# Optimization experiments

Measured on AMD Instinct MI355X. Metric: run time of the kernel, lower is better.

Reference implementation:

```python
import jax, jax.numpy as jnp
import numpy as np

B, S, E, H, DK, DV, DF = 4, 2048, 512, 8, 64, 64, 2048
EPS = 1e-3  # keras LayerNormalization default epsilon


def setup_inputs() -> dict:
    key = jax.random.key(0)
    ks = jax.random.split(key, 24)
    def n(k, shape, scale=0.02):
        return jax.random.normal(k, shape, jnp.float32) * scale
    inp = {}
    inp["x"] = jax.random.normal(ks[0], (B, S, E), jnp.float32)
    inp["encoder_output"] = jax.random.normal(ks[1], (B, S, E), jnp.float32)
    # lookahead mask: 1 above the diagonal (masked), broadcast over batch/heads
    inp["lookahead_mask"] = jnp.triu(jnp.ones((S, S), jnp.int32), k=1)[None, None]
    # padding mask: 0 = keep (no padding in this synthetic batch)
    inp["padding_mask"] = jnp.zeros((B, 1, 1, S), jnp.int32)
    # self-attention params
    inp["sa_Wq"] = n(ks[2], (E, H * DK)); inp["sa_bq"] = jnp.zeros((H * DK,), jnp.float32)
    inp["sa_Wk"] = n(ks[3], (E, H * DK)); inp["sa_bk"] = jnp.zeros((H * DK,), jnp.float32)
    inp["sa_Wv"] = n(ks[4], (E, H * DV)); inp["sa_bv"] = jnp.zeros((H * DV,), jnp.float32)
    inp["sa_Wo"] = n(ks[5], (H * DV, E)); inp["sa_bo"] = jnp.zeros((E,), jnp.float32)
    # cross-attention params
    inp["ca_Wq"] = n(ks[6], (E, H * DK)); inp["ca_bq"] = jnp.zeros((H * DK,), jnp.float32)
    inp["ca_Wk"] = n(ks[7], (E, H * DK)); inp["ca_bk"] = jnp.zeros((H * DK,), jnp.float32)
    inp["ca_Wv"] = n(ks[8], (E, H * DV)); inp["ca_bv"] = jnp.zeros((H * DV,), jnp.float32)
    inp["ca_Wo"] = n(ks[9], (H * DV, E)); inp["ca_bo"] = jnp.zeros((E,), jnp.float32)
    # feed-forward params
    inp["ff_W1"] = n(ks[10], (E, DF)); inp["ff_b1"] = jnp.zeros((DF,), jnp.float32)
    inp["ff_W2"] = n(ks[11], (DF, E)); inp["ff_b2"] = jnp.zeros((E,), jnp.float32)
    # layernorm params (3 add&norm blocks)
    for i in (1, 2, 3):
        inp[f"ln{i}_g"] = jnp.ones((E,), jnp.float32)
        inp[f"ln{i}_b"] = jnp.zeros((E,), jnp.float32)
    return inp


def _mha(q_in, k_in, v_in, mask, Wq, bq, Wk, bk, Wv, bv, Wo, bo):
    Bq, Sq, _ = q_in.shape
    Sk = k_in.shape[1]
    q = (q_in @ Wq + bq).reshape(Bq, Sq, H, DK).transpose(0, 2, 1, 3)  # bhqd
    k = (k_in @ Wk + bk).reshape(Bq, Sk, H, DK).transpose(0, 2, 1, 3)  # bhkd
    v = (v_in @ Wv + bv).reshape(Bq, Sk, H, DV).transpose(0, 2, 1, 3)  # bhkd
    scores = jnp.einsum("bhqd,bhkd->bhqk", q, k) / jnp.sqrt(jnp.float32(DK))
    scores = scores - 1e9 * mask.astype(scores.dtype)  # additive mask (1 = masked)
    attn = jax.nn.softmax(scores, axis=-1)
    out = jnp.einsum("bhqk,bhkd->bhqd", attn, v)
    out = out.transpose(0, 2, 1, 3).reshape(Bq, Sq, H * DV)
    return out @ Wo + bo


def _add_norm(x, sub, g, b):
    y = x + sub
    m = jnp.mean(y, axis=-1, keepdims=True)
    v = jnp.var(y, axis=-1, keepdims=True)
    return (y - m) / jnp.sqrt(v + EPS) * g + b


def reference(x, encoder_output, lookahead_mask, padding_mask,
              sa_Wq, sa_bq, sa_Wk, sa_bk, sa_Wv, sa_bv, sa_Wo, sa_bo,
              ca_Wq, ca_bq, ca_Wk, ca_bk, ca_Wv, ca_bv, ca_Wo, ca_bo,
              ff_W1, ff_b1, ff_W2, ff_b2,
              ln1_g, ln1_b, ln2_g, ln2_b, ln3_g, ln3_b):
    # dropout is identity at inference (training=False)
    a1 = _mha(x, x, x, lookahead_mask,
              sa_Wq, sa_bq, sa_Wk, sa_bk, sa_Wv, sa_bv, sa_Wo, sa_bo)
    x1 = _add_norm(x, a1, ln1_g, ln1_b)
    a2 = _mha(x1, encoder_output, encoder_output, padding_mask,
              ca_Wq, ca_bq, ca_Wk, ca_bk, ca_Wv, ca_bv, ca_Wo, ca_bo)
    x2 = _add_norm(x1, a2, ln2_g, ln2_b)
    ff = jax.nn.relu(x2 @ ff_W1 + ff_b1) @ ff_W2 + ff_b2
    return _add_norm(x2, ff, ln3_g, ln3_b)
```

## Files before the change

kernel.cpp:

```cpp
#include <hip/hip_runtime.h>

#define Bx  4
#define Sx  2048
#define Ex  512
#define Hx  8
#define Tt  (Bx * Sx)

typedef short          short8 __attribute__((ext_vector_type(8)));
typedef float          f32x4  __attribute__((ext_vector_type(4)));
typedef unsigned short u16;

__device__ __forceinline__ u16 f2bf(float f) {
    unsigned int u = __float_as_uint(f);
    u += 0x7fffu + ((u >> 16) & 1u);
    return (u16)(u >> 16);
}
__device__ __forceinline__ float bf2f(u16 h) {
    return __uint_as_float(((unsigned int)h) << 16);
}

__global__ __launch_bounds__(256) void f32_to_bf16_2(const float* __restrict__ a,
                                                     const float* __restrict__ b,
                                                     u16* __restrict__ oa,
                                                     u16* __restrict__ ob)
{
    const float* in  = blockIdx.y ? b : a;
    u16*         out = blockIdx.y ? ob : oa;
    int i = (blockIdx.x * 256 + threadIdx.x) << 2;
    float4 v = *(const float4*)(in + i);
    ushort4 o;
    o.x = f2bf(v.x); o.y = f2bf(v.y); o.z = f2bf(v.z); o.w = f2bf(v.w);
    *(ushort4*)(out + i) = o;
}

__global__ __launch_bounds__(256) void transpose_bf16(const float* __restrict__ W,
                                                      u16* __restrict__ Wt,
                                                      int K, int N)
{
    __shared__ u16 tile[32][33];
    const int n0 = blockIdx.x * 32, k0 = blockIdx.y * 32;
    const int tx = threadIdx.x & 31, ty = threadIdx.x >> 5;
#pragma unroll
    for (int i = 0; i < 32; i += 8)
        tile[ty + i][tx] = f2bf(W[(size_t)(k0 + ty + i) * N + n0 + tx]);
    __syncthreads();
#pragma unroll
    for (int i = 0; i < 32; i += 8)
        Wt[(size_t)(n0 + ty + i) * K + k0 + tx] = tile[tx][ty + i];
}

struct WPtrs { const float* w[8]; };
__global__ __launch_bounds__(256) void transpose8_bf16(WPtrs ws, u16* __restrict__ base)
{
    __shared__ u16 tile[32][33];
    const float* W  = ws.w[blockIdx.z];
    u16*         Wt = base + (size_t)blockIdx.z * 262144;
    const int n0 = blockIdx.x * 32, k0 = blockIdx.y * 32;
    const int tx = threadIdx.x & 31, ty = threadIdx.x >> 5;
#pragma unroll
    for (int i = 0; i < 32; i += 8)
        tile[ty + i][tx] = f2bf(W[(size_t)(k0 + ty + i) * 512 + n0 + tx]);
    __syncthreads();
#pragma unroll
    for (int i = 0; i < 32; i += 8)
        Wt[(size_t)(n0 + ty + i) * 512 + k0 + tx] = tile[tx][ty + i];
}

template<int OUT_BF16, int RELU>
__global__ __launch_bounds__(256) void gemm128(const u16* __restrict__ A,
                                               const u16* __restrict__ Bt,
                                               const float* __restrict__ b0,
                                               const float* __restrict__ b1,
                                               const float* __restrict__ b2,
                                               const float* __restrict__ b3,
                                               void* __restrict__ Cout,
                                               int M, int N, int K, int ldc)
{
    __shared__ u16 As[128 * 40];
    __shared__ u16 Bs[128 * 40];

    const int tid  = threadIdx.x;
    const int w    = tid >> 6;
    const int lane = tid & 63;
    const int c    = lane & 15;
    const int quad = lane >> 4;
    const int wr   = w >> 1, wc = w & 1;
    const int m0   = blockIdx.y * 128;
    const int n0   = blockIdx.x * 128;

    const int row0 = tid >> 2;
    const int kc   = (tid & 3) << 3;

    const u16* Ap = A  + (size_t)(m0 + row0) * K + kc;
    const u16* Bp = Bt + (size_t)(n0 + row0) * K + kc;
    const size_t rstep = (size_t)64 * K;

    f32x4 acc[4][4];
#pragma unroll
    for (int i = 0; i < 4; i++)
#pragma unroll
        for (int j = 0; j < 4; j++) { acc[i][j][0]=0.f; acc[i][j][1]=0.f; acc[i][j][2]=0.f; acc[i][j][3]=0.f; }

    short8 ra0 = *(const short8*)(Ap);
    short8 ra1 = *(const short8*)(Ap + rstep);
    short8 rb0 = *(const short8*)(Bp);
    short8 rb1 = *(const short8*)(Bp + rstep);

    for (int k0 = 0; k0 < K; k0 += 32) {
        __syncthreads();
        *(short8*)&As[row0 * 40 + kc]        = ra0;
        *(short8*)&As[(row0 + 64) * 40 + kc] = ra1;
        *(short8*)&Bs[row0 * 40 + kc]        = rb0;
        *(short8*)&Bs[(row0 + 64) * 40 + kc] = rb1;
        __syncthreads();

        if (k0 + 32 < K) {
            ra0 = *(const short8*)(Ap + k0 + 32);
            ra1 = *(const short8*)(Ap + rstep + k0 + 32);
            rb0 = *(const short8*)(Bp + k0 + 32);
            rb1 = *(const short8*)(Bp + rstep + k0 + 32);
        }

        short8 af[4], bf[4];
#pragma unroll
        for (int i = 0; i < 4; i++)
            af[i] = *(const short8*)&As[(wr * 64 + i * 16 + c) * 40 + quad * 8];
#pragma unroll
        for (int j = 0; j < 4; j++)
            bf[j] = *(const short8*)&Bs[(wc * 64 + j * 16 + c) * 40 + quad * 8];
#pragma unroll
        for (int i = 0; i < 4; i++)
#pragma unroll
            for (int j = 0; j < 4; j++)
                acc[i][j] = __builtin_amdgcn_mfma_f32_16x16x32_bf16(af[i], bf[j], acc[i][j], 0, 0, 0);
    }

    const int seg = n0 >> 9;
    const float* bp = seg == 0 ? b0 : (seg == 1 ? b1 : (seg == 2 ? b2 : b3));
    const int nbase = n0 & 511;
    float bv[4];
#pragma unroll
    for (int j = 0; j < 4; j++) bv[j] = bp[nbase + wc * 64 + j * 16 + c];

#pragma unroll
    for (int i = 0; i < 4; i++) {
#pragma unroll
        for (int j = 0; j < 4; j++) {
            int colg = n0 + wc * 64 + j * 16 + c;
#pragma unroll
            for (int r = 0; r < 4; r++) {
                int rowg = m0 + wr * 64 + i * 16 + quad * 4 + r;
                float v = acc[i][j][r] + bv[j];
                if (RELU) v = fmaxf(v, 0.f);
                if (OUT_BF16) ((u16*)Cout)[(size_t)rowg * ldc + colg] = f2bf(v);
                else          ((float*)Cout)[(size_t)rowg * ldc + colg] = v;
            }
        }
    }
}

template<int OUT_BF16, int RELU>
__global__ __launch_bounds__(128) void gemm64(const u16* __restrict__ A,
                                              const u16* __restrict__ Bt,
                                              const float* __restrict__ bias,
                                              void* __restrict__ Cout,
                                              int M, int N, int K, int ldc)
{
    __shared__ u16 As[128 * 40];
    __shared__ u16 Bs[64 * 40];

    const int tid  = threadIdx.x;
    const int w    = tid >> 6;
    const int lane = tid & 63;
    const int c    = lane & 15;
    const int quad = lane >> 4;
    const int m0   = blockIdx.y * 128;
    const int n0   = blockIdx.x * 64;

    const int rA = tid >> 2;
    const int kc = (tid & 3) << 3;

    const u16* Ap = A  + (size_t)(m0 + rA) * K + kc;
    const u16* Bp = Bt + (size_t)(n0 + rA) * K + kc;
    const size_t a32 = (size_t)32 * K;

    f32x4 acc[4][4];
#pragma unroll
    for (int i = 0; i < 4; i++)
#pragma unroll
        for (int j = 0; j < 4; j++) { acc[i][j][0]=0.f; acc[i][j][1]=0.f; acc[i][j][2]=0.f; acc[i][j][3]=0.f; }

    short8 ra[4], rb[2];
#pragma unroll
    for (int i = 0; i < 4; i++) ra[i] = *(const short8*)(Ap + i * a32);
#pragma unroll
    for (int i = 0; i < 2; i++) rb[i] = *(const short8*)(Bp + i * a32);

    for (int k0 = 0; k0 < K; k0 += 32) {
        __syncthreads();
#pragma unroll
        for (int i = 0; i < 4; i++) *(short8*)&As[(rA + i * 32) * 40 + kc] = ra[i];
#pragma unroll
        for (int i = 0; i < 2; i++) *(short8*)&Bs[(rA + i * 32) * 40 + kc] = rb[i];
        __syncthreads();

        if (k0 + 32 < K) {
#pragma unroll
            for (int i = 0; i < 4; i++) ra[i] = *(const short8*)(Ap + i * a32 + k0 + 32);
#pragma unroll
            for (int i = 0; i < 2; i++) rb[i] = *(const short8*)(Bp + i * a32 + k0 + 32);
        }

        short8 af[4], bf[4];
#pragma unroll
        for (int i = 0; i < 4; i++)
            af[i] = *(const short8*)&As[(w * 64 + i * 16 + c) * 40 + quad * 8];
#pragma unroll
        for (int j = 0; j < 4; j++)
            bf[j] = *(const short8*)&Bs[(j * 16 + c) * 40 + quad * 8];
#pragma unroll
        for (int i = 0; i < 4; i++)
#pragma unroll
            for (int j = 0; j < 4; j++)
                acc[i][j] = __builtin_amdgcn_mfma_f32_16x16x32_bf16(af[i], bf[j], acc[i][j], 0, 0, 0);
    }

    float bv[4];
#pragma unroll
    for (int j = 0; j < 4; j++) bv[j] = bias[n0 + j * 16 + c];

#pragma unroll
    for (int i = 0; i < 4; i++) {
#pragma unroll
        for (int j = 0; j < 4; j++) {
            int colg = n0 + j * 16 + c;
#pragma unroll
            for (int r = 0; r < 4; r++) {
                int rowg = m0 + w * 64 + i * 16 + quad * 4 + r;
                float v = acc[i][j][r] + bv[j];
                if (RELU) v = fmaxf(v, 0.f);
                if (OUT_BF16) ((u16*)Cout)[(size_t)rowg * ldc + colg] = f2bf(v);
                else          ((float*)Cout)[(size_t)rowg * ldc + colg] = v;
            }
        }
    }
}

template<bool CAUSAL>
__global__ __launch_bounds__(256) void attn_mfma(const u16* __restrict__ Q,
                                                 const u16* __restrict__ K,
                                                 const u16* __restrict__ V,
                                                 u16* __restrict__ O,
                                                 int ldq, int ldk, int ldv)
{
    __shared__ u16          Klds[32 * 72];
    __shared__ u16          Vtlds[64 * 40];
    __shared__ unsigned int Plds[4][16 * 19];

    const int tid  = threadIdx.x;
    const int w    = tid >> 6;
    const int lane = tid & 63;
    const int c    = lane & 15;
    const int quad = lane >> 4;

    const int flat = blockIdx.y * 32 + blockIdx.x;
    const int idx  = flat >> 3;
    const int bh   = (flat & 7) * 4 + (idx >> 5);
    const int q0   = (idx & 31) * 64;

    const int b    = bh >> 3;
    const int h    = bh & 7;
    const int bS   = b * Sx;
    const int hoff = h * 64;
    const int qw   = q0 + w * 16;

    const int kkey = tid >> 3;
    const int kc8  = (tid & 7) << 3;
    const int vdim = tid & 63;
    const int vp   = (tid >> 6) << 3;

    short8 qa[2];
    {
        const u16* qp = Q + (size_t)(bS + qw + c) * ldq + hoff;
        qa[0] = *(const short8*)(qp + quad * 8);
        qa[1] = *(const short8*)(qp + 32 + quad * 8);
    }

    f32x4 of[4];
#pragma unroll
    for (int f = 0; f < 4; f++) { of[f][0]=0.f; of[f][1]=0.f; of[f][2]=0.f; of[f][3]=0.f; }
    float lpart[4] = {0.f, 0.f, 0.f, 0.f};

    const int kend = CAUSAL ? (q0 + 64) : Sx;

    const u16* Kgp = K + (size_t)(bS + kkey) * ldk + hoff + kc8;
    const u16* Vgp = V + (size_t)bS * ldv + hoff + vdim;

    short8 kr = *(const short8*)(Kgp);
    union { short8 v; u16 u[8]; } vb;
#pragma unroll
    for (int j = 0; j < 8; j++) {
        int pos = vp + j;
        int key = (pos >> 1) + ((pos & 1) << 4);
        vb.u[j] = Vgp[(size_t)key * ldv];
    }

    for (int kt = 0; kt < kend; kt += 32) {
        __syncthreads();
        *(short8*)&Klds[kkey * 72 + kc8] = kr;
        *(short8*)&Vtlds[vdim * 40 + vp] = vb.v;
        __syncthreads();

        if (kt + 32 < kend) {
            kr = *(const short8*)(Kgp + (size_t)(kt + 32) * ldk);
#pragma unroll
            for (int j = 0; j < 8; j++) {
                int pos = vp + j;
                int key = kt + 32 + (pos >> 1) + ((pos & 1) << 4);
                vb.u[j] = Vgp[(size_t)key * ldv];
            }
        }

        int fmax = 2;
        if (CAUSAL) {
            int d = ((qw + 15 - kt) >> 4) + 1;
            fmax = d < 2 ? d : 2;
        }

        if (fmax > 0) {
            f32x4 s[2];
#pragma unroll
            for (int f = 0; f < 2; f++) {
                if (f < fmax) {
                    short8 kb0 = *(const short8*)&Klds[(f * 16 + c) * 72 + quad * 8];
                    short8 kb1 = *(const short8*)&Klds[(f * 16 + c) * 72 + 32 + quad * 8];
                    f32x4 z; z[0]=0.f; z[1]=0.f; z[2]=0.f; z[3]=0.f;
                    z = __builtin_amdgcn_mfma_f32_16x16x32_bf16(qa[0], kb0, z, 0, 0, 0);
                    z = __builtin_amdgcn_mfma_f32_16x16x32_bf16(qa[1], kb1, z, 0, 0, 0);
                    s[f] = z;
                }
            }

#pragma unroll
            for (int r = 0; r < 4; r++) {
                int qg = qw + quad * 4 + r;
                float p0 = 0.f, p1 = 0.f;
                if (!(CAUSAL && (kt + c) > qg))
                    p0 = __expf(s[0][r] * 0.125f);
                if (fmax > 1 && !(CAUSAL && (kt + 16 + c) > qg))
                    p1 = __expf(s[1][r] * 0.125f);
                u16 b0 = f2bf(p0), b1 = f2bf(p1);
                lpart[r] += bf2f(b0) + bf2f(b1);
                *(volatile unsigned int*)&Plds[w][(quad * 4 + r) * 19 + c] =
                    (unsigned int)b0 | ((unsigned int)b1 << 16);
            }

            union { unsigned int u[4]; short8 s8; } pu;
#pragma unroll
            for (int i = 0; i < 4; i++)
                pu.u[i] = *(volatile const unsigned int*)&Plds[w][c * 19 + quad * 4 + i];
            short8 pa = pu.s8;

#pragma unroll
            for (int f2 = 0; f2 < 4; f2++) {
                short8 vbf = *(const short8*)&Vtlds[(f2 * 16 + c) * 40 + quad * 8];
                of[f2] = __builtin_amdgcn_mfma_f32_16x16x32_bf16(pa, vbf, of[f2], 0, 0, 0);
            }
        }
    }

#pragma unroll
    for (int r = 0; r < 4; r++) {
        float v = lpart[r];
        v += __shfl_xor(v, 1, 64);
        v += __shfl_xor(v, 2, 64);
        v += __shfl_xor(v, 4, 64);
        v += __shfl_xor(v, 8, 64);
        lpart[r] = 1.f / v;
    }

    u16* Ob = O + (size_t)(bS + qw) * Ex + hoff;
#pragma unroll
    for (int f = 0; f < 4; f++)
#pragma unroll
        for (int r = 0; r < 4; r++)
            Ob[(size_t)(quad * 4 + r) * Ex + f * 16 + c] = f2bf(of[f][r] * lpart[r]);
}

__global__ __launch_bounds__(256) void ln_add(const float* __restrict__ x,
                                              const float* __restrict__ s,
                                              const float* __restrict__ g,
                                              const float* __restrict__ bta,
                                              float* __restrict__ out,
                                              u16* __restrict__ out_bf)
{
    __shared__ float red[8];
    const int    row  = blockIdx.x;
    const int    t    = threadIdx.x;
    const size_t base = (size_t)row * Ex;

    float2 xv = *(const float2*)(x + base + (t << 1));
    float2 sv = *(const float2*)(s + base + (t << 1));
    float  y0 = xv.x + sv.x;
    float  y1 = xv.y + sv.y;

    float sum = y0 + y1;
    float sq  = y0 * y0 + y1 * y1;
#pragma unroll
    for (int o = 32; o > 0; o >>= 1) {
        sum += __shfl_down(sum, o, 64);
        sq  += __shfl_down(sq,  o, 64);
    }
    const int wid = t >> 6, lane = t & 63;
    if (lane == 0) { red[wid] = sum; red[4 + wid] = sq; }
    __syncthreads();
    if (t == 0) {
        red[0] = red[0] + red[1] + red[2] + red[3];
        red[4] = red[4] + red[5] + red[6] + red[7];
    }
    __syncthreads();

    const float mean = red[0] * (1.f / 512.f);
    const float var  = red[4] * (1.f / 512.f) - mean * mean;
    const float rstd = rsqrtf(var + 1e-3f);

    float2 gv = *(const float2*)(g   + (t << 1));
    float2 bv = *(const float2*)(bta + (t << 1));
    float  o0 = (y0 - mean) * rstd * gv.x + bv.x;
    float  o1 = (y1 - mean) * rstd * gv.y + bv.y;
    *(float2*)(out + base + (t << 1)) = make_float2(o0, o1);
    if (out_bf) {
        ushort2 ob; ob.x = f2bf(o0); ob.y = f2bf(o1);
        *(ushort2*)(out_bf + base + (t << 1)) = ob;
    }
}

extern "C" void kernel_launch(void* const* d_in, const int* in_sizes, int n_in,
                              void* d_out, int out_size, void* d_ws, size_t ws_size,
                              hipStream_t stream)
{
    const float* x     = (const float*)d_in[0];
    const float* enc   = (const float*)d_in[1];
    const float* sa_Wq = (const float*)d_in[4],  *sa_bq = (const float*)d_in[5];
    const float* sa_Wk = (const float*)d_in[6],  *sa_bk = (const float*)d_in[7];
    const float* sa_Wv = (const float*)d_in[8],  *sa_bv = (const float*)d_in[9];
    const float* sa_Wo = (const float*)d_in[10], *sa_bo = (const float*)d_in[11];
    const float* ca_Wq = (const float*)d_in[12], *ca_bq = (const float*)d_in[13];
    const float* ca_Wk = (const float*)d_in[14], *ca_bk = (const float*)d_in[15];
    const float* ca_Wv = (const float*)d_in[16], *ca_bv = (const float*)d_in[17];
    const float* ca_Wo = (const float*)d_in[18], *ca_bo = (const float*)d_in[19];
    const float* ff_W1 = (const float*)d_in[20], *ff_b1 = (const float*)d_in[21];
    const float* ff_W2 = (const float*)d_in[22], *ff_b2 = (const float*)d_in[23];
    const float* ln1_g = (const float*)d_in[24], *ln1_b = (const float*)d_in[25];
    const float* ln2_g = (const float*)d_in[26], *ln2_b = (const float*)d_in[27];
    const float* ln3_g = (const float*)d_in[28], *ln3_b = (const float*)d_in[29];

    char* ws = (char*)d_ws;
    const size_t MB = 1024 * 1024;
    u16*   bw   = (u16*)(ws);
    u16*   xb   = (u16*)(ws + 8  * MB);
    u16*   encb = (u16*)(ws + 16 * MB);
    u16*   qkvB = (u16*)(ws + 24 * MB);
    u16*   qb   = (u16*)(ws + 24 * MB);
    u16*   kvB  = (u16*)(ws + 32 * MB);
    u16*   ff1b = (u16*)(ws + 24 * MB);
    u16*   ob   = (u16*)(ws + 48 * MB);
    float* projF= (float*)(ws + 56 * MB);
    float* x1f  = (float*)(ws + 72 * MB);
    u16*   x1b  = (u16*)(ws + 88 * MB);
    u16*   x2b  = (u16*)(ws + 88 * MB);
    float* x2f  = (float*)(ws + 8  * MB);

    u16* wsaq = bw;
    u16* wsao = bw + 786432;
    u16* wcaq = bw + 1048576;
    u16* wcak = bw + 1310720;
    u16* wcao = bw + 1835008;
    u16* wff1 = bw + 2097152;
    u16* wff2 = bw + 3145728;

    f32_to_bf16_2<<<dim3(Tt * Ex / 1024, 2), dim3(256), 0, stream>>>(x, enc, xb, encb);
    WPtrs wp; wp.w[0]=sa_Wq; wp.w[1]=sa_Wk; wp.w[2]=sa_Wv; wp.w[3]=sa_Wo;
    wp.w[4]=ca_Wq; wp.w[5]=ca_Wk; wp.w[6]=ca_Wv; wp.w[7]=ca_Wo;
    transpose8_bf16<<<dim3(16, 16, 8), dim3(256), 0, stream>>>(wp, bw);
    transpose_bf16<<<dim3(64, 16), dim3(256), 0, stream>>>(ff_W1, wff1, 512, 2048);
    transpose_bf16<<<dim3(16, 64), dim3(256), 0, stream>>>(ff_W2, wff2, 2048, 512);

    auto G128 = [&](const u16* A, const u16* Wt, const float* b0, const float* b1,
                    const float* b2, const float* b3, void* C,
                    int N, int K, int ldc, int out_bf, int relu) {
        dim3 grid(N / 128, Tt / 128);
        if (out_bf) {
            if (relu) gemm128<1,1><<<grid, dim3(256), 0, stream>>>(A, Wt, b0,b1,b2,b3, C, Tt, N, K, ldc);
            else      gemm128<1,0><<<grid, dim3(256), 0, stream>>>(A, Wt, b0,b1,b2,b3, C, Tt, N, K, ldc);
        } else        gemm128<0,0><<<grid, dim3(256), 0, stream>>>(A, Wt, b0,b1,b2,b3, C, Tt, N, K, ldc);
    };
    auto G64 = [&](const u16* A, const u16* Wt, const float* bi, void* C,
                   int K, int ldc, int out_bf) {
        dim3 grid(512 / 64, Tt / 128);
        if (out_bf) gemm64<1,0><<<grid, dim3(128), 0, stream>>>(A, Wt, bi, C, Tt, 512, K, ldc);
        else        gemm64<0,0><<<grid, dim3(128), 0, stream>>>(A, Wt, bi, C, Tt, 512, K, ldc);
    };
    const dim3 agrid(Sx / 64, Bx * Hx);

    G128(xb, wsaq, sa_bq, sa_bk, sa_bv, sa_bv, qkvB, 1536, 512, 1536, 1, 0);
    attn_mfma<true><<<agrid, dim3(256), 0, stream>>>(qkvB, qkvB + 512, qkvB + 1024,
                                                     ob, 1536, 1536, 1536);
    G64(ob, wsao, sa_bo, projF, 512, 512, 0);
    ln_add<<<dim3(Tt), dim3(256), 0, stream>>>(x, projF, ln1_g, ln1_b, x1f, x1b);

    G64(x1b, wcaq, ca_bq, qb, 512, 512, 1);
    G128(encb, wcak, ca_bk, ca_bv, ca_bv, ca_bv, kvB, 1024, 512, 1024, 1, 0);
    attn_mfma<false><<<agrid, dim3(256), 0, stream>>>(qb, kvB, kvB + 512,
                                                      ob, 512, 1024, 1024);
    G64(ob, wcao, ca_bo, projF, 512, 512, 0);
    ln_add<<<dim3(Tt), dim3(256), 0, stream>>>(x1f, projF, ln2_g, ln2_b, x2f, x2b);

    G128(x2b, wff1, ff_b1, ff_b1 + 512, ff_b1 + 1024, ff_b1 + 1536,
         ff1b, 2048, 512, 2048, 1, 1);
    G64(ff1b, wff2, ff_b2, projF, 2048, 512, 0);
    ln_add<<<dim3(Tt), dim3(256), 0, stream>>>(x2f, projF, ln3_g, ln3_b,
                                               (float*)d_out, (u16*)nullptr);
}
```

Before: 534.9 us.

## Double query rows per attention block to reuse K/V tiles across two subtiles

Each wave in the attention kernel now handles 32 query rows as two 16-row subtiles, so a block covers 128 queries instead of 64 and the grid is halved. Each K/V tile loaded into LDS, and each K fragment read into registers, is reused by twice as many query rows, which cuts global and LDS traffic per unit of work. The cost is more registers per thread (two sets of output accumulators, a larger P buffer in LDS) and fewer blocks, which may lower occupancy. In the causal case the larger blocks also make the load across blocks less even.

```diff
diff --git a/kernel.cpp b/kernel.cpp
--- a/kernel.cpp
+++ b/kernel.cpp
@@ -255,7 +255,7 @@
 {
     __shared__ u16          Klds[32 * 72];
     __shared__ u16          Vtlds[64 * 40];
-    __shared__ unsigned int Plds[4][16 * 19];
+    __shared__ unsigned int Plds[4][32 * 19];
 
     const int tid  = threadIdx.x;
     const int w    = tid >> 6;
@@ -263,35 +263,38 @@
     const int c    = lane & 15;
     const int quad = lane >> 4;
 
-    const int flat = blockIdx.y * 32 + blockIdx.x;
+    const int flat = blockIdx.y * 16 + blockIdx.x;
     const int idx  = flat >> 3;
-    const int bh   = (flat & 7) * 4 + (idx >> 5);
-    const int q0   = (idx & 31) * 64;
+    const int bh   = (flat & 7) * 4 + (idx >> 4);
+    const int q0   = (idx & 15) * 128;
 
     const int b    = bh >> 3;
     const int h    = bh & 7;
     const int bS   = b * Sx;
     const int hoff = h * 64;
-    const int qw   = q0 + w * 16;
+    const int qw   = q0 + w * 32;
 
     const int kkey = tid >> 3;
     const int kc8  = (tid & 7) << 3;
     const int vdim = tid & 63;
     const int vp   = (tid >> 6) << 3;
 
-    short8 qa[2];
-    {
-        const u16* qp = Q + (size_t)(bS + qw + c) * ldq + hoff;
-        qa[0] = *(const short8*)(qp + quad * 8);
-        qa[1] = *(const short8*)(qp + 32 + quad * 8);
-    }
-
-    f32x4 of[4];
-#pragma unroll
-    for (int f = 0; f < 4; f++) { of[f][0]=0.f; of[f][1]=0.f; of[f][2]=0.f; of[f][3]=0.f; }
-    float lpart[4] = {0.f, 0.f, 0.f, 0.f};
-
-    const int kend = CAUSAL ? (q0 + 64) : Sx;
+    short8 qa[2][2];
+#pragma unroll
+    for (int a = 0; a < 2; a++) {
+        const u16* qp = Q + (size_t)(bS + qw + a * 16 + c) * ldq + hoff;
+        qa[a][0] = *(const short8*)(qp + quad * 8);
+        qa[a][1] = *(const short8*)(qp + 32 + quad * 8);
+    }
+
+    f32x4 of[2][4];
+#pragma unroll
+    for (int a = 0; a < 2; a++)
+#pragma unroll
+        for (int f = 0; f < 4; f++) { of[a][f][0]=0.f; of[a][f][1]=0.f; of[a][f][2]=0.f; of[a][f][3]=0.f; }
+    float lpart[2][4] = {{0.f,0.f,0.f,0.f},{0.f,0.f,0.f,0.f}};
+
+    const int kend = CAUSAL ? (q0 + 128) : Sx;
 
     const u16* Kgp = K + (size_t)(bS + kkey) * ldk + hoff + kc8;
     const u16* Vgp = V + (size_t)bS * ldv + hoff + vdim;
@@ -321,70 +324,100 @@
             }
         }
 
-        int fmax = 2;
+        int fm0 = 2, fm1 = 2;
         if (CAUSAL) {
-            int d = ((qw + 15 - kt) >> 4) + 1;
-            fmax = d < 2 ? d : 2;
-        }
-
-        if (fmax > 0) {
-            f32x4 s[2];
+            int d0 = ((qw + 15 - kt) >> 4) + 1;
+            int d1 = ((qw + 31 - kt) >> 4) + 1;
+            fm0 = d0 < 2 ? d0 : 2;
+            fm1 = d1 < 2 ? d1 : 2;
+        }
+
+        if (fm1 > 0) {
+            short8 kb[2][2];
 #pragma unroll
             for (int f = 0; f < 2; f++) {
-                if (f < fmax) {
-                    short8 kb0 = *(const short8*)&Klds[(f * 16 + c) * 72 + quad * 8];
-                    short8 kb1 = *(const short8*)&Klds[(f * 16 + c) * 72 + 32 + quad * 8];
-                    f32x4 z; z[0]=0.f; z[1]=0.f; z[2]=0.f; z[3]=0.f;
-                    z = __builtin_amdgcn_mfma_f32_16x16x32_bf16(qa[0], kb0, z, 0, 0, 0);
-                    z = __builtin_amdgcn_mfma_f32_16x16x32_bf16(qa[1], kb1, z, 0, 0, 0);
-                    s[f] = z;
+                if (f < fm1) {
+                    kb[f][0] = *(const short8*)&Klds[(f * 16 + c) * 72 + quad * 8];
+                    kb[f][1] = *(const short8*)&Klds[(f * 16 + c) * 72 + 32 + quad * 8];
                 }
             }
 
-#pragma unroll
-            for (int r = 0; r < 4; r++) {
-                int qg = qw + quad * 4 + r;
-                float p0 = 0.f, p1 = 0.f;
-                if (!(CAUSAL && (kt + c) > qg))
-                    p0 = __expf(s[0][r] * 0.125f);
-                if (fmax > 1 && !(CAUSAL && (kt + 16 + c) > qg))
-                    p1 = __expf(s[1][r] * 0.125f);
-                u16 b0 = f2bf(p0), b1 = f2bf(p1);
-                lpart[r] += bf2f(b0) + bf2f(b1);
-                *(volatile unsigned int*)&Plds[w][(quad * 4 + r) * 19 + c] =
-                    (unsigned int)b0 | ((unsigned int)b1 << 16);
-            }
-
-            union { unsigned int u[4]; short8 s8; } pu;
+            f32x4 s[2][2];
+#pragma unroll
+            for (int a = 0; a < 2; a++) {
+                const int fma_ = a ? fm1 : fm0;
+#pragma unroll
+                for (int f = 0; f < 2; f++) {
+                    if (f < fma_) {
+                        f32x4 z; z[0]=0.f; z[1]=0.f; z[2]=0.f; z[3]=0.f;
+                        z = __builtin_amdgcn_mfma_f32_16x16x32_bf16(qa[a][0], kb[f][0], z, 0, 0, 0);
+                        z = __builtin_amdgcn_mfma_f32_16x16x32_bf16(qa[a][1], kb[f][1], z, 0, 0, 0);
+                        s[a][f] = z;
+                    }
+                }
+            }
+
+#pragma unroll
+            for (int a = 0; a < 2; a++) {
+                const int fma_ = a ? fm1 : fm0;
+                if (fma_ > 0) {
+#pragma unroll
+                    for (int r = 0; r < 4; r++) {
+                        int qg = qw + a * 16 + quad * 4 + r;
+                        float p0 = 0.f, p1 = 0.f;
+                        if (!(CAUSAL && (kt + c) > qg))
+                            p0 = __expf(s[a][0][r] * 0.125f);
+                        if (fma_ > 1 && !(CAUSAL && (kt + 16 + c) > qg))
+                            p1 = __expf(s[a][1][r] * 0.125f);
+                        u16 b0 = f2bf(p0), b1 = f2bf(p1);
+                        lpart[a][r] += bf2f(b0) + bf2f(b1);
+                        *(volatile unsigned int*)&Plds[w][(a * 16 + quad * 4 + r) * 19 + c] =
+                            (unsigned int)b0 | ((unsigned int)b1 << 16);
+                    }
+                }
+            }
+
+            union { unsigned int u[4]; short8 s8; } pu0, pu1;
+            if (fm0 > 0) {
+#pragma unroll
+                for (int i = 0; i < 4; i++)
+                    pu0.u[i] = *(volatile const unsigned int*)&Plds[w][c * 19 + quad * 4 + i];
+            }
 #pragma unroll
             for (int i = 0; i < 4; i++)
-                pu.u[i] = *(volatile const unsigned int*)&Plds[w][c * 19 + quad * 4 + i];
-            short8 pa = pu.s8;
+                pu1.u[i] = *(volatile const unsigned int*)&Plds[w][(16 + c) * 19 + quad * 4 + i];
 
 #pragma unroll
             for (int f2 = 0; f2 < 4; f2++) {
                 short8 vbf = *(const short8*)&Vtlds[(f2 * 16 + c) * 40 + quad * 8];
-                of[f2] = __builtin_amdgcn_mfma_f32_16x16x32_bf16(pa, vbf, of[f2], 0, 0, 0);
-            }
-        }
-    }
-
-#pragma unroll
-    for (int r = 0; r < 4; r++) {
-        float v = lpart[r];
-        v += __shfl_xor(v, 1, 64);
-        v += __shfl_xor(v, 2, 64);
-        v += __shfl_xor(v, 4, 64);
-        v += __shfl_xor(v, 8, 64);
-        lpart[r] = 1.f / v;
-    }
+                if (fm0 > 0)
+                    of[0][f2] = __builtin_amdgcn_mfma_f32_16x16x32_bf16(pu0.s8, vbf, of[0][f2], 0, 0, 0);
+                of[1][f2] = __builtin_amdgcn_mfma_f32_16x16x32_bf16(pu1.s8, vbf, of[1][f2], 0, 0, 0);
+            }
+        }
+    }
+
+#pragma unroll
+    for (int a = 0; a < 2; a++)
+#pragma unroll
+        for (int r = 0; r < 4; r++) {
+            float v = lpart[a][r];
+            v += __shfl_xor(v, 1, 64);
+            v += __shfl_xor(v, 2, 64);
+            v += __shfl_xor(v, 4, 64);
+            v += __shfl_xor(v, 8, 64);
+            lpart[a][r] = 1.f / v;
+        }
 
     u16* Ob = O + (size_t)(bS + qw) * Ex + hoff;
 #pragma unroll
-    for (int f = 0; f < 4; f++)
-#pragma unroll
-        for (int r = 0; r < 4; r++)
-            Ob[(size_t)(quad * 4 + r) * Ex + f * 16 + c] = f2bf(of[f][r] * lpart[r]);
+    for (int a = 0; a < 2; a++)
+#pragma unroll
+        for (int f = 0; f < 4; f++)
+#pragma unroll
+            for (int r = 0; r < 4; r++)
+                Ob[(size_t)(a * 16 + quad * 4 + r) * Ex + f * 16 + c] =
+                    f2bf(of[a][f][r] * lpart[a][r]);
 }
 
 __global__ __launch_bounds__(256) void ln_add(const float* __restrict__ x,
@@ -501,7 +534,7 @@
         if (out_bf) gemm64<1,0><<<grid, dim3(128), 0, stream>>>(A, Wt, bi, C, Tt, 512, K, ldc);
         else        gemm64<0,0><<<grid, dim3(128), 0, stream>>>(A, Wt, bi, C, Tt, 512, K, ldc);
     };
-    const dim3 agrid(Sx / 64, Bx * Hx);
+    const dim3 agrid(Sx / 128, Bx * Hx);
 
     G128(xb, wsaq, sa_bq, sa_bk, sa_bv, sa_bv, qkvB, 1536, 512, 1536, 1, 0);
     attn_mfma<true><<<agrid, dim3(256), 0, stream>>>(qkvB, qkvB + 512, qkvB + 1024,
```

Result: slower. 569.2 us (+6.4%).

## Double-buffer K/V tiles and keep P in registers via transposed score MFMA

Applied to the files above, without the earlier changes.

The attention kernel now double-buffers the K and transposed-V tiles in LDS, writing the next tile after compute so each step needs one barrier instead of two. It also swaps the MFMA operand order for QK^T so the score fragment lands already laid out as the A operand for PV. That removes the per-wave P round-trip through LDS, and the V key permutation is adjusted to match. Row sums are reduced across quads and redistributed with shuffles. LDS use grows for the second buffer, and the new layout has to stay consistent between the score, probability and V fragments.

```diff
diff --git a/kernel.cpp b/kernel.cpp
--- a/kernel.cpp
+++ b/kernel.cpp
@@ -253,9 +253,8 @@
                                                  u16* __restrict__ O,
                                                  int ldq, int ldk, int ldv)
 {
-    __shared__ u16          Klds[32 * 72];
-    __shared__ u16          Vtlds[64 * 40];
-    __shared__ unsigned int Plds[4][16 * 19];
+    __shared__ u16 Klds[2][32 * 72];
+    __shared__ u16 Vtlds[2][64 * 40];
 
     const int tid  = threadIdx.x;
     const int w    = tid >> 6;
@@ -277,7 +276,11 @@
     const int kkey = tid >> 3;
     const int kc8  = (tid & 7) << 3;
     const int vdim = tid & 63;
-    const int vp   = (tid >> 6) << 3;
+    const int vq   = tid >> 6;
+    const int vp   = vq << 3;
+    int vkey[8];
+#pragma unroll
+    for (int j = 0; j < 8; j++) vkey[j] = ((j & 4) << 2) + (vq << 2) + (j & 3);
 
     short8 qa[2];
     {
@@ -289,102 +292,104 @@
     f32x4 of[4];
 #pragma unroll
     for (int f = 0; f < 4; f++) { of[f][0]=0.f; of[f][1]=0.f; of[f][2]=0.f; of[f][3]=0.f; }
-    float lpart[4] = {0.f, 0.f, 0.f, 0.f};
+    float lpart = 0.f;
 
     const int kend = CAUSAL ? (q0 + 64) : Sx;
 
     const u16* Kgp = K + (size_t)(bS + kkey) * ldk + hoff + kc8;
     const u16* Vgp = V + (size_t)bS * ldv + hoff + vdim;
 
-    short8 kr = *(const short8*)(Kgp);
-    union { short8 v; u16 u[8]; } vb;
-#pragma unroll
-    for (int j = 0; j < 8; j++) {
-        int pos = vp + j;
-        int key = (pos >> 1) + ((pos & 1) << 4);
-        vb.u[j] = Vgp[(size_t)key * ldv];
-    }
-
+    {
+        short8 kr = *(const short8*)(Kgp);
+        union { short8 v; u16 u[8]; } vb;
+#pragma unroll
+        for (int j = 0; j < 8; j++) vb.u[j] = Vgp[(size_t)vkey[j] * ldv];
+        *(short8*)&Klds[0][kkey * 72 + kc8] = kr;
+        *(short8*)&Vtlds[0][vdim * 40 + vp] = vb.v;
+    }
+    __syncthreads();
+
+    int cur = 0;
     for (int kt = 0; kt < kend; kt += 32) {
-        __syncthreads();
-        *(short8*)&Klds[kkey * 72 + kc8] = kr;
-        *(short8*)&Vtlds[vdim * 40 + vp] = vb.v;
-        __syncthreads();
-
-        if (kt + 32 < kend) {
+        const bool more = (kt + 32 < kend);
+
+        short8 kr;
+        union { short8 v; u16 u[8]; } vb;
+        if (more) {
             kr = *(const short8*)(Kgp + (size_t)(kt + 32) * ldk);
 #pragma unroll
-            for (int j = 0; j < 8; j++) {
-                int pos = vp + j;
-                int key = kt + 32 + (pos >> 1) + ((pos & 1) << 4);
-                vb.u[j] = Vgp[(size_t)key * ldv];
-            }
-        }
-
-        int fmax = 2;
+            for (int j = 0; j < 8; j++)
+                vb.u[j] = Vgp[(size_t)(kt + 32 + vkey[j]) * ldv];
+        }
+
+        int fm = 2;
         if (CAUSAL) {
             int d = ((qw + 15 - kt) >> 4) + 1;
-            fmax = d < 2 ? d : 2;
-        }
-
-        if (fmax > 0) {
+            fm = d < 2 ? d : 2;
+        }
+
+        if (fm > 0) {
             f32x4 s[2];
 #pragma unroll
             for (int f = 0; f < 2; f++) {
-                if (f < fmax) {
-                    short8 kb0 = *(const short8*)&Klds[(f * 16 + c) * 72 + quad * 8];
-                    short8 kb1 = *(const short8*)&Klds[(f * 16 + c) * 72 + 32 + quad * 8];
+                if (f < fm) {
+                    short8 kb0 = *(const short8*)&Klds[cur][(f * 16 + c) * 72 + quad * 8];
+                    short8 kb1 = *(const short8*)&Klds[cur][(f * 16 + c) * 72 + 32 + quad * 8];
                     f32x4 z; z[0]=0.f; z[1]=0.f; z[2]=0.f; z[3]=0.f;
-                    z = __builtin_amdgcn_mfma_f32_16x16x32_bf16(qa[0], kb0, z, 0, 0, 0);
-                    z = __builtin_amdgcn_mfma_f32_16x16x32_bf16(qa[1], kb1, z, 0, 0, 0);
+                    z = __builtin_amdgcn_mfma_f32_16x16x32_bf16(kb0, qa[0], z, 0, 0, 0);
+                    z = __builtin_amdgcn_mfma_f32_16x16x32_bf16(kb1, qa[1], z, 0, 0, 0);
                     s[f] = z;
                 }
             }
 
-#pragma unroll
-            for (int r = 0; r < 4; r++) {
-                int qg = qw + quad * 4 + r;
-                float p0 = 0.f, p1 = 0.f;
-                if (!(CAUSAL && (kt + c) > qg))
-                    p0 = __expf(s[0][r] * 0.125f);
-                if (fmax > 1 && !(CAUSAL && (kt + 16 + c) > qg))
-                    p1 = __expf(s[1][r] * 0.125f);
-                u16 b0 = f2bf(p0), b1 = f2bf(p1);
-                lpart[r] += bf2f(b0) + bf2f(b1);
-                *(volatile unsigned int*)&Plds[w][(quad * 4 + r) * 19 + c] =
-                    (unsigned int)b0 | ((unsigned int)b1 << 16);
+            const int qg = qw + c;
+            union { unsigned int u[4]; short8 s8; } pa;
+#pragma unroll
+            for (int f = 0; f < 2; f++) {
+                u16 pb[4];
+#pragma unroll
+                for (int r = 0; r < 4; r++) {
+                    float p = 0.f;
+                    int kg = kt + f * 16 + quad * 4 + r;
+                    if (f < fm && !(CAUSAL && kg > qg))
+                        p = __expf(s[f][r] * 0.125f);
+                    pb[r] = f2bf(p);
+                    lpart += bf2f(pb[r]);
+                }
+                pa.u[f * 2 + 0] = (unsigned int)pb[0] | ((unsigned int)pb[1] << 16);
+                pa.u[f * 2 + 1] = (unsigned int)pb[2] | ((unsigned int)pb[3] << 16);
             }
 
-            union { unsigned int u[4]; short8 s8; } pu;
-#pragma unroll
-            for (int i = 0; i < 4; i++)
-                pu.u[i] = *(volatile const unsigned int*)&Plds[w][c * 19 + quad * 4 + i];
-            short8 pa = pu.s8;
-
 #pragma unroll
             for (int f2 = 0; f2 < 4; f2++) {
-                short8 vbf = *(const short8*)&Vtlds[(f2 * 16 + c) * 40 + quad * 8];
-                of[f2] = __builtin_amdgcn_mfma_f32_16x16x32_bf16(pa, vbf, of[f2], 0, 0, 0);
+                short8 vbf = *(const short8*)&Vtlds[cur][(f2 * 16 + c) * 40 + quad * 8];
+                of[f2] = __builtin_amdgcn_mfma_f32_16x16x32_bf16(pa.s8, vbf, of[f2], 0, 0, 0);
             }
         }
-    }
-
-#pragma unroll
-    for (int r = 0; r < 4; r++) {
-        float v = lpart[r];
-        v += __shfl_xor(v, 1, 64);
-        v += __shfl_xor(v, 2, 64);
-        v += __shfl_xor(v, 4, 64);
-        v += __shfl_xor(v, 8, 64);
-        lpart[r] = 1.f / v;
-    }
+
+        if (more) {
+            *(short8*)&Klds[cur ^ 1][kkey * 72 + kc8] = kr;
+            *(short8*)&Vtlds[cur ^ 1][vdim * 40 + vp] = vb.v;
+        }
+        __syncthreads();
+        cur ^= 1;
+    }
+
+    float D = lpart;
+    D += __shfl_xor(D, 16, 64);
+    D += __shfl_xor(D, 32, 64);
+    float rcp = 1.f / D;
+    float rinv[4];
+#pragma unroll
+    for (int r = 0; r < 4; r++)
+        rinv[r] = __shfl(rcp, quad * 4 + r, 64);
 
     u16* Ob = O + (size_t)(bS + qw) * Ex + hoff;
 #pragma unroll
     for (int f = 0; f < 4; f++)
 #pragma unroll
         for (int r = 0; r < 4; r++)
-            Ob[(size_t)(quad * 4 + r) * Ex + f * 16 + c] = f2bf(of[f][r] * lpart[r]);
+            Ob[(size_t)(quad * 4 + r) * Ex + f * 16 + c] = f2bf(of[f][r] * rinv[r]);
 }
 
 __global__ __launch_bounds__(256) void ln_add(const float* __restrict__ x,
```

Measured after the change: 507.3 us. 1.05x faster.
